# Kernel tuning notes

Measured on AMD Instinct MI355X. Metric: run time of the kernel, lower is better.

The kernel has to match this reference:

```python
import jax, jax.numpy as jnp
import numpy as np

NB_HEAD = 4
SIZE_PER_HEAD = 50
D_MODEL = 200
B, S = 4, 4096


def setup_inputs() -> dict:
    key = jax.random.key(0)
    ks = jax.random.split(key, 7)
    q = jax.random.normal(ks[0], (B, S, D_MODEL), dtype=jnp.float32)
    k = jax.random.normal(ks[1], (B, S, D_MODEL), dtype=jnp.float32)
    v = jax.random.normal(ks[2], (B, S, D_MODEL), dtype=jnp.float32)
    # glorot-uniform-like init for weights
    def glorot(key, shape):
        lim = jnp.sqrt(6.0 / (shape[0] + shape[1])).astype(jnp.float32)
        return jax.random.uniform(key, shape, jnp.float32, -lim, lim)
    WQ = glorot(ks[3], (D_MODEL, SIZE_PER_HEAD))
    WK = glorot(ks[4], (D_MODEL, SIZE_PER_HEAD))
    WV = glorot(ks[5], (D_MODEL, SIZE_PER_HEAD))
    WO = glorot(ks[6], (NB_HEAD * SIZE_PER_HEAD, D_MODEL))
    return {"q": q, "k": k, "v": v, "WQ": WQ, "WK": WK, "WV": WV, "WO": WO}


def reference(q, k, v, WQ, WK, WV, WO):
    # The original per-head loop reuses the SAME WQ/WK/WV each iteration,
    # so every head output is identical. Compute attention once and tile.
    Qp = jnp.einsum('bsd,de->bse', q, WQ)  # [B,S,h]
    Kp = jnp.einsum('bsd,de->bse', k, WK)
    Vp = jnp.einsum('bsd,de->bse', v, WV)
    scale = 1.0 / jnp.sqrt(jnp.asarray(SIZE_PER_HEAD, dtype=Qp.dtype))
    A = jax.nn.softmax(jnp.einsum('bqe,bke->bqk', Qp, Kp) * scale, axis=-1)  # [B,S,S]
    O = jnp.einsum('bqk,bke->bqe', A, Vp)  # [B,S,h]
    O_concat = jnp.tile(O, (1, 1, NB_HEAD))  # [B,S,NB_HEAD*h]
    return jnp.einsum('bsf,fd->bsd', O_concat, WO)
```

## Files before the change

### kernel.cpp

```cpp
#include <hip/hip_runtime.h>
#include <hip/hip_bf16.h>


typedef short s4 __attribute__((ext_vector_type(4)));
typedef float f4 __attribute__((ext_vector_type(4)));

#define SLEN 4096
#define NB 4
#define DMODEL 200
#define HREAL 50
#define HP 64
#define DMP 208
#define KVB 64
#define QSCALE 0.20402789f

__device__ __forceinline__ short f2bf(float f) {
  unsigned u = __builtin_bit_cast(unsigned, f);
  u += 0x7FFFu + ((u >> 16) & 1u);
  return (short)(u >> 16);
}

__device__ __forceinline__ float fexp2(float x) { return __builtin_amdgcn_exp2f(x); }

__global__ void prep_weights(const float* __restrict__ WQ, const float* __restrict__ WK,
                             const float* __restrict__ WV, const float* __restrict__ WO,
                             short* __restrict__ wqt, short* __restrict__ wkt,
                             short* __restrict__ wvt, short* __restrict__ wot) {
  int id = blockIdx.x * 256 + threadIdx.x;
  const int NW = HP * DMP;
  if (id < 3 * NW) {
    int which = id / NW, rem = id % NW;
    int e = rem / DMP, d = rem % DMP;
    float v = 0.f;
    if (e < HREAL && d < DMODEL) {
      const float* W = (which == 0) ? WQ : (which == 1 ? WK : WV);
      v = W[d * HREAL + e];
      if (which == 0) v *= QSCALE;
    }
    short* T = (which == 0) ? wqt : (which == 1 ? wkt : wvt);
    T[e * DMP + d] = f2bf(v);
  } else if (id < 4 * NW) {
    int rem = id - 3 * NW;
    int dm = rem / HP, e = rem % HP;
    float v = 0.f;
    if (dm < DMODEL && e < HREAL) {
      v = WO[(e)*DMODEL + dm] + WO[(HREAL + e) * DMODEL + dm] +
          WO[(2 * HREAL + e) * DMODEL + dm] + WO[(3 * HREAL + e) * DMODEL + dm];
    }
    wot[dm * HP + e] = f2bf(v);
  }
}

__global__ __launch_bounds__(256) void proj_kernel(
    const float* __restrict__ q, const float* __restrict__ k, const float* __restrict__ v,
    const short* __restrict__ wqt, const short* __restrict__ wkt, const short* __restrict__ wvt,
    short* __restrict__ Qp, short* __restrict__ Kp, short* __restrict__ VpT) {
  const int mode = blockIdx.z;
  const float* X = (mode == 0) ? q : (mode == 1 ? k : v);
  const short* WT = (mode == 0) ? wqt : (mode == 1 ? wkt : wvt);
  const int lane = threadIdx.x & 63, wid = threadIdx.x >> 6;
  const int l15 = lane & 15, g = lane >> 4;
  const int sbase = blockIdx.x * 64 + wid * 16;
  const int row = sbase + l15;
  f4 acc[4] = {};
  for (int c = 0; c < 13; ++c) {
    int d0 = 16 * c + 4 * g;
    f4 a4 = {};
    if (d0 < DMODEL) a4 = *(const f4*)(X + (size_t)row * DMODEL + d0);
    s4 af;
#pragma unroll
    for (int j = 0; j < 4; ++j) af[j] = f2bf(a4[j]);
#pragma unroll
    for (int n = 0; n < 4; ++n) {
      s4 bf = *(const s4*)(WT + (16 * n + l15) * DMP + d0);
      acc[n] = __builtin_amdgcn_mfma_f32_16x16x16bf16_1k(af, bf, acc[n], 0, 0, 0);
    }
  }
  if (mode < 2) {
    short* OUT = (mode == 0) ? Qp : Kp;
#pragma unroll
    for (int n = 0; n < 4; ++n)
#pragma unroll
      for (int r = 0; r < 4; ++r) {
        int rr = sbase + 4 * g + r;
        OUT[rr * HP + 16 * n + l15] = f2bf(acc[n][r]);
      }
  } else {
#pragma unroll
    for (int n = 0; n < 4; ++n)
#pragma unroll
      for (int r = 0; r < 4; ++r) {
        int rr = sbase + 4 * g + r;
        int bb = rr >> 12, s = rr & 4095;
        VpT[((bb * HP) + 16 * n + l15) * SLEN + s] = f2bf(acc[n][r]);
      }
  }
}

__global__ __launch_bounds__(256, 4) void attn_kernel(
    const short* __restrict__ Qp, const short* __restrict__ Kp,
    const short* __restrict__ VpT, float* __restrict__ Mp,
    float* __restrict__ Lp, float* __restrict__ Op) {
  __shared__ __align__(16) char Klds[KVB * 128];
  __shared__ __align__(16) char Vlds[HP * 128];
  const int tid = threadIdx.x;
  const int lane = tid & 63, wid = tid >> 6;
  const int l15 = lane & 15, g = lane >> 4;
  const int b = blockIdx.y, z = blockIdx.z;
  const int nsplit = gridDim.z;
  const int qrowA = blockIdx.x * 128 + wid * 32 + l15;
  const int qrowB = qrowA + 16;
  const int ksw = (l15 & 7) << 4;

  s4 qfA[4], qfB[4];
  {
    const short* qpa = Qp + (size_t)(b * SLEN + qrowA) * HP + 4 * g;
    const short* qpb = Qp + (size_t)(b * SLEN + qrowB) * HP + 4 * g;
#pragma unroll
    for (int c = 0; c < 4; ++c) {
      qfA[c] = *(const s4*)(qpa + 16 * c);
      qfB[c] = *(const s4*)(qpb + 16 * c);
    }
  }

  const int kr0 = l15 * 128 + ((8 * g) ^ ksw);
  const int kr1 = l15 * 128 + ((32 + 8 * g) ^ ksw);
  const int kr2 = l15 * 128 + ((64 + 8 * g) ^ ksw);
  const int kr3 = l15 * 128 + ((96 + 8 * g) ^ ksw);
  const int vb = l15 * 128 + ((8 * g) ^ ksw);

  const int cj0 = tid, cj1 = tid + 256;
  const int ci0 = (cj0 ^ ((cj0 >> 3) & 7)) * 16;
  const int ci1 = (cj1 ^ ((cj1 >> 3) & 7)) * 16;
  const int d0 = cj0 >> 3, d1 = cj1 >> 3;
  const int ch0 = ((cj0 & 7) ^ (d0 & 7)) * 16;
  const int ch1 = ((cj1 & 7) ^ (d1 & 7)) * 16;

  const int kv0 = z * (SLEN / nsplit);
  const char* kp0 = (const char*)Kp + (size_t)(b * SLEN + kv0) * 128 + ci0;
  const char* kp1 = (const char*)Kp + (size_t)(b * SLEN + kv0) * 128 + ci1;
  const char* vp0 =
      (const char*)VpT + ((size_t)(b * HP + d0) * SLEN + kv0) * 2 + ch0;
  const char* vp1 =
      (const char*)VpT + ((size_t)(b * HP + d1) * SLEN + kv0) * 2 + ch1;

  f4 rk0 = *(const f4*)kp0;
  f4 rk1 = *(const f4*)kp1;
  f4 rv0 = *(const f4*)vp0;
  f4 rv1 = *(const f4*)vp1;
  kp0 += KVB * 128;
  kp1 += KVB * 128;
  vp0 += KVB * 2;
  vp1 += KVB * 2;

  f4 oA[4] = {}, oB[4] = {};
  float mA = -1e30f, lsumA = 0.f;
  float mB = -1e30f, lsumB = 0.f;
  const int nsteps = SLEN / nsplit / KVB;
  for (int step = 0; step < nsteps; ++step) {
    __syncthreads();
    *(f4*)(Klds + tid * 16) = rk0;
    *(f4*)(Klds + tid * 16 + 4096) = rk1;
    *(f4*)(Vlds + tid * 16) = rv0;
    *(f4*)(Vlds + tid * 16 + 4096) = rv1;
    __syncthreads();
    if (step + 1 < nsteps) {
      rk0 = *(const f4*)kp0;
      rk1 = *(const f4*)kp1;
      rv0 = *(const f4*)vp0;
      rv1 = *(const f4*)vp1;
      kp0 += KVB * 128;
      kp1 += KVB * 128;
      vp0 += KVB * 2;
      vp1 += KVB * 2;
    }
#pragma unroll
    for (int tt = 0; tt < 4; ++tt) {
      f4 stA = {}, stB = {};
      {
        s4 kf0 = *(const s4*)(Klds + kr0 + tt * 2048);
        s4 kf1 = *(const s4*)(Klds + kr1 + tt * 2048);
        s4 kf2 = *(const s4*)(Klds + kr2 + tt * 2048);
        s4 kf3 = *(const s4*)(Klds + kr3 + tt * 2048);
        __builtin_amdgcn_s_setprio(1);
        stA = __builtin_amdgcn_mfma_f32_16x16x16bf16_1k(kf0, qfA[0], stA, 0, 0, 0);
        stB = __builtin_amdgcn_mfma_f32_16x16x16bf16_1k(kf0, qfB[0], stB, 0, 0, 0);
        stA = __builtin_amdgcn_mfma_f32_16x16x16bf16_1k(kf1, qfA[1], stA, 0, 0, 0);
        stB = __builtin_amdgcn_mfma_f32_16x16x16bf16_1k(kf1, qfB[1], stB, 0, 0, 0);
        stA = __builtin_amdgcn_mfma_f32_16x16x16bf16_1k(kf2, qfA[2], stA, 0, 0, 0);
        stB = __builtin_amdgcn_mfma_f32_16x16x16bf16_1k(kf2, qfB[2], stB, 0, 0, 0);
        stA = __builtin_amdgcn_mfma_f32_16x16x16bf16_1k(kf3, qfA[3], stA, 0, 0, 0);
        stB = __builtin_amdgcn_mfma_f32_16x16x16bf16_1k(kf3, qfB[3], stB, 0, 0, 0);
        __builtin_amdgcn_s_setprio(0);
      }
      float tmaxA = fmaxf(fmaxf(stA[0], stA[1]), fmaxf(stA[2], stA[3]));
      if (__builtin_expect(__any(tmaxA > mA + 8.0f), 0)) {
        float t = fmaxf(tmaxA, __shfl_xor(tmaxA, 16));
        t = fmaxf(t, __shfl_xor(t, 32));
        t = fmaxf(t, mA);
        float corr = fexp2(mA - t);
        lsumA *= corr;
#pragma unroll
        for (int n = 0; n < 4; ++n) {
          oA[n][0] *= corr; oA[n][1] *= corr; oA[n][2] *= corr; oA[n][3] *= corr;
        }
        mA = t;
      }
      float pa0 = fexp2(stA[0] - mA), pa1 = fexp2(stA[1] - mA);
      float pa2 = fexp2(stA[2] - mA), pa3 = fexp2(stA[3] - mA);
      lsumA += (pa0 + pa1) + (pa2 + pa3);
      union { unsigned u[2]; s4 s; } puA;
      asm("v_cvt_pk_bf16_f32 %0, %1, %2" : "=v"(puA.u[0]) : "v"(pa0), "v"(pa1));
      asm("v_cvt_pk_bf16_f32 %0, %1, %2" : "=v"(puA.u[1]) : "v"(pa2), "v"(pa3));
      s4 pfA = puA.s;
      float tmaxB = fmaxf(fmaxf(stB[0], stB[1]), fmaxf(stB[2], stB[3]));
      if (__builtin_expect(__any(tmaxB > mB + 8.0f), 0)) {
        float t = fmaxf(tmaxB, __shfl_xor(tmaxB, 16));
        t = fmaxf(t, __shfl_xor(t, 32));
        t = fmaxf(t, mB);
        float corr = fexp2(mB - t);
        lsumB *= corr;
#pragma unroll
        for (int n = 0; n < 4; ++n) {
          oB[n][0] *= corr; oB[n][1] *= corr; oB[n][2] *= corr; oB[n][3] *= corr;
        }
        mB = t;
      }
      float pb0 = fexp2(stB[0] - mB), pb1 = fexp2(stB[1] - mB);
      float pb2 = fexp2(stB[2] - mB), pb3 = fexp2(stB[3] - mB);
      lsumB += (pb0 + pb1) + (pb2 + pb3);
      union { unsigned u[2]; s4 s; } puB;
      asm("v_cvt_pk_bf16_f32 %0, %1, %2" : "=v"(puB.u[0]) : "v"(pb0), "v"(pb1));
      asm("v_cvt_pk_bf16_f32 %0, %1, %2" : "=v"(puB.u[1]) : "v"(pb2), "v"(pb3));
      s4 pfB = puB.s;
      const char* vrow = Vlds + (vb ^ (tt << 5));
      __builtin_amdgcn_s_setprio(1);
#pragma unroll
      for (int n = 0; n < 4; ++n) {
        s4 vf = *(const s4*)(vrow + n * 2048);
        oA[n] = __builtin_amdgcn_mfma_f32_16x16x16bf16_1k(vf, pfA, oA[n], 0, 0, 0);
        oB[n] = __builtin_amdgcn_mfma_f32_16x16x16bf16_1k(vf, pfB, oB[n], 0, 0, 0);
      }
      __builtin_amdgcn_s_setprio(0);
    }
  }
  lsumA += __shfl_xor(lsumA, 16);
  lsumA += __shfl_xor(lsumA, 32);
  lsumB += __shfl_xor(lsumB, 16);
  lsumB += __shfl_xor(lsumB, 32);
  const int rowgA = b * SLEN + qrowA;
  const int rowgB = b * SLEN + qrowB;
  const int NR = NB * SLEN;
  if (lane < 16) {
    Mp[z * NR + rowgA] = mA;
    Lp[z * NR + rowgA] = lsumA;
    Mp[z * NR + rowgB] = mB;
    Lp[z * NR + rowgB] = lsumB;
  }
  float* opA = Op + ((size_t)z * NR + rowgA) * HP;
  float* opB = Op + ((size_t)z * NR + rowgB) * HP;
#pragma unroll
  for (int n = 0; n < 4; ++n) {
    *(f4*)(opA + 16 * n + 4 * g) = oA[n];
    *(f4*)(opB + 16 * n + 4 * g) = oB[n];
  }
}

template <int NSPLIT>
__global__ __launch_bounds__(256) void combineproj_kernel(
    const float* __restrict__ Mp, const float* __restrict__ Lp,
    const float* __restrict__ Op, const short* __restrict__ wot,
    float* __restrict__ out) {
  const int lane = threadIdx.x & 63, wid = threadIdx.x >> 6;
  const int l15 = lane & 15, g = lane >> 4;
  const int sbase = blockIdx.x * 64 + wid * 16;
  const int row = sbase + l15;
  const int NR = NB * SLEN;
  float mm = -1e30f;
#pragma unroll
  for (int s = 0; s < NSPLIT; ++s) mm = fmaxf(mm, Mp[s * NR + row]);
  float w[NSPLIT];
  float L = 0.f;
#pragma unroll
  for (int s = 0; s < NSPLIT; ++s) {
    w[s] = fexp2(Mp[s * NR + row] - mm);
    L += w[s] * Lp[s * NR + row];
  }
  float inv = 1.0f / L;
  s4 af[4];
#pragma unroll
  for (int c = 0; c < 4; ++c) {
    f4 acc = {};
#pragma unroll
    for (int s = 0; s < NSPLIT; ++s) {
      f4 vv = *(const f4*)(Op + ((size_t)s * NR + row) * HP + 16 * c + 4 * g);
      acc[0] += w[s] * vv[0];
      acc[1] += w[s] * vv[1];
      acc[2] += w[s] * vv[2];
      acc[3] += w[s] * vv[3];
    }
#pragma unroll
    for (int r = 0; r < 4; ++r) af[c][r] = f2bf(acc[r] * inv);
  }
  for (int n = 0; n < 13; ++n) {
    f4 acc = {};
    const short* brow = wot + (16 * n + l15) * HP + 4 * g;
#pragma unroll
    for (int c = 0; c < 4; ++c) {
      s4 bf = *(const s4*)(brow + 16 * c);
      acc = __builtin_amdgcn_mfma_f32_16x16x16bf16_1k(af[c], bf, acc, 0, 0, 0);
    }
    int dm = 16 * n + l15;
    if (dm < DMODEL) {
#pragma unroll
      for (int r = 0; r < 4; ++r) {
        int rr = sbase + 4 * g + r;
        out[(size_t)rr * DMODEL + dm] = acc[r];
      }
    }
  }
}

extern "C" void kernel_launch(void* const* d_in, const int* in_sizes, int n_in,
                              void* d_out, int out_size, void* d_ws, size_t ws_size,
                              hipStream_t stream) {
  const float* q = (const float*)d_in[0];
  const float* k = (const float*)d_in[1];
  const float* v = (const float*)d_in[2];
  const float* WQ = (const float*)d_in[3];
  const float* WK = (const float*)d_in[4];
  const float* WV = (const float*)d_in[5];
  const float* WO = (const float*)d_in[6];
  float* out = (float*)d_out;
  char* ws = (char*)d_ws;

  const size_t MB2 = 2097152;
  const size_t NR = (size_t)NB * SLEN;
  size_t need8 = 131072 + 4 * MB2 + 8 * NR * 4 * 2 + 8 * NR * HP * 4;
  int nsplit = (ws_size >= need8) ? 8 : 4;

  short* wqt = (short*)(ws + 0);
  short* wkt = (short*)(ws + 32768);
  short* wvt = (short*)(ws + 65536);
  short* wot = (short*)(ws + 98304);
  short* Qp = (short*)(ws + 131072);
  short* Kp = (short*)(ws + 131072 + MB2);
  short* VpT = (short*)(ws + 131072 + 2 * MB2);
  float* Mp = (float*)(ws + 131072 + 4 * MB2);
  float* Lp = Mp + nsplit * NR;
  float* Op = Lp + nsplit * NR;

  prep_weights<<<dim3(208), dim3(256), 0, stream>>>(WQ, WK, WV, WO, wqt, wkt, wvt, wot);
  proj_kernel<<<dim3(256, 1, 3), dim3(256), 0, stream>>>(q, k, v, wqt, wkt, wvt, Qp, Kp, VpT);
  attn_kernel<<<dim3(32, NB, nsplit), dim3(256), 0, stream>>>(Qp, Kp, VpT, Mp, Lp, Op);
  if (nsplit == 8)
    combineproj_kernel<8><<<dim3(256), dim3(256), 0, stream>>>(Mp, Lp, Op, wot, out);
  else
    combineproj_kernel<4><<<dim3(256), dim3(256), 0, stream>>>(Mp, Lp, Op, wot, out);
}
```

Baseline: 73.21 us.

## Double-buffer K/V tiles in LDS to drop one barrier per step

Splits the K and V shared-memory tiles into two buffers. Each step computes on one buffer and writes the prefetched next tile into the other after compute, which needs only one __syncthreads per step instead of two. This doubles LDS use to 32KB per block, which may limit occupancy at the 4-blocks launch bound. The global loads are also held in registers across the whole compute phase.

```diff
diff --git a/kernel.cpp b/kernel.cpp
--- a/kernel.cpp
+++ b/kernel.cpp
@@ -101,8 +101,8 @@
     const short* __restrict__ Qp, const short* __restrict__ Kp,
     const short* __restrict__ VpT, float* __restrict__ Mp,
     float* __restrict__ Lp, float* __restrict__ Op) {
-  __shared__ __align__(16) char Klds[KVB * 128];
-  __shared__ __align__(16) char Vlds[HP * 128];
+  __shared__ __align__(16) char Klds[2][KVB * 128];
+  __shared__ __align__(16) char Vlds[2][HP * 128];
   const int tid = threadIdx.x;
   const int lane = tid & 63, wid = tid >> 6;
   const int l15 = lane & 15, g = lane >> 4;
@@ -144,27 +144,30 @@
   const char* vp1 =
       (const char*)VpT + ((size_t)(b * HP + d1) * SLEN + kv0) * 2 + ch1;
 
-  f4 rk0 = *(const f4*)kp0;
-  f4 rk1 = *(const f4*)kp1;
-  f4 rv0 = *(const f4*)vp0;
-  f4 rv1 = *(const f4*)vp1;
-  kp0 += KVB * 128;
-  kp1 += KVB * 128;
-  vp0 += KVB * 2;
-  vp1 += KVB * 2;
+  {
+    f4 k0 = *(const f4*)kp0;
+    f4 k1 = *(const f4*)kp1;
+    f4 v0 = *(const f4*)vp0;
+    f4 v1 = *(const f4*)vp1;
+    *(f4*)(Klds[0] + tid * 16) = k0;
+    *(f4*)(Klds[0] + tid * 16 + 4096) = k1;
+    *(f4*)(Vlds[0] + tid * 16) = v0;
+    *(f4*)(Vlds[0] + tid * 16 + 4096) = v1;
+    kp0 += KVB * 128;
+    kp1 += KVB * 128;
+    vp0 += KVB * 2;
+    vp1 += KVB * 2;
+  }
 
   f4 oA[4] = {}, oB[4] = {};
   float mA = -1e30f, lsumA = 0.f;
   float mB = -1e30f, lsumB = 0.f;
   const int nsteps = SLEN / nsplit / KVB;
   for (int step = 0; step < nsteps; ++step) {
-    __syncthreads();
-    *(f4*)(Klds + tid * 16) = rk0;
-    *(f4*)(Klds + tid * 16 + 4096) = rk1;
-    *(f4*)(Vlds + tid * 16) = rv0;
-    *(f4*)(Vlds + tid * 16 + 4096) = rv1;
-    __syncthreads();
-    if (step + 1 < nsteps) {
+    const int p = step & 1;
+    f4 rk0, rk1, rv0, rv1;
+    const bool more = (step + 1 < nsteps);
+    if (more) {
       rk0 = *(const f4*)kp0;
       rk1 = *(const f4*)kp1;
       rv0 = *(const f4*)vp0;
@@ -174,14 +177,17 @@
       vp0 += KVB * 2;
       vp1 += KVB * 2;
     }
+    __syncthreads();
+    const char* Kbuf = Klds[p];
+    const char* Vbuf = Vlds[p];
 #pragma unroll
     for (int tt = 0; tt < 4; ++tt) {
       f4 stA = {}, stB = {};
       {
-        s4 kf0 = *(const s4*)(Klds + kr0 + tt * 2048);
-        s4 kf1 = *(const s4*)(Klds + kr1 + tt * 2048);
-        s4 kf2 = *(const s4*)(Klds + kr2 + tt * 2048);
-        s4 kf3 = *(const s4*)(Klds + kr3 + tt * 2048);
+        s4 kf0 = *(const s4*)(Kbuf + kr0 + tt * 2048);
+        s4 kf1 = *(const s4*)(Kbuf + kr1 + tt * 2048);
+        s4 kf2 = *(const s4*)(Kbuf + kr2 + tt * 2048);
+        s4 kf3 = *(const s4*)(Kbuf + kr3 + tt * 2048);
         __builtin_amdgcn_s_setprio(1);
         stA = __builtin_amdgcn_mfma_f32_16x16x16bf16_1k(kf0, qfA[0], stA, 0, 0, 0);
         stB = __builtin_amdgcn_mfma_f32_16x16x16bf16_1k(kf0, qfB[0], stB, 0, 0, 0);
@@ -233,7 +239,7 @@
       asm("v_cvt_pk_bf16_f32 %0, %1, %2" : "=v"(puB.u[0]) : "v"(pb0), "v"(pb1));
       asm("v_cvt_pk_bf16_f32 %0, %1, %2" : "=v"(puB.u[1]) : "v"(pb2), "v"(pb3));
       s4 pfB = puB.s;
-      const char* vrow = Vlds + (vb ^ (tt << 5));
+      const char* vrow = Vbuf + (vb ^ (tt << 5));
       __builtin_amdgcn_s_setprio(1);
 #pragma unroll
       for (int n = 0; n < 4; ++n) {
@@ -242,6 +248,12 @@
         oB[n] = __builtin_amdgcn_mfma_f32_16x16x16bf16_1k(vf, pfB, oB[n], 0, 0, 0);
       }
       __builtin_amdgcn_s_setprio(0);
+    }
+    if (more) {
+      *(f4*)(Klds[p ^ 1] + tid * 16) = rk0;
+      *(f4*)(Klds[p ^ 1] + tid * 16 + 4096) = rk1;
+      *(f4*)(Vlds[p ^ 1] + tid * 16) = rv0;
+      *(f4*)(Vlds[p ^ 1] + tid * 16 + 4096) = rv1;
     }
   }
   lsumA += __shfl_xor(lsumA, 16);
```

After: 72.21 us. No clear change (-1.4%).
